# Kernel optimization log

Measured on AMD Instinct MI355X. Metric: run time of the kernel, lower is better.

## Reference

```python
import jax, jax.numpy as jnp
import numpy as np
import math

B, C, H, W = 8, 512, 32, 32
NUM_GROUPS = 32
NUM_HEADS = C // 64  # num_head_channels=64 -> 8 heads
EPS = 1e-5


def setup_inputs() -> dict:
    key = jax.random.key(0)
    ks = jax.random.split(key, 7)
    x = jax.random.normal(ks[0], (B, C, H, W), dtype=jnp.float32)
    gn_w = jax.random.uniform(ks[1], (C,), dtype=jnp.float32, minval=0.5, maxval=1.5)
    gn_b = jax.random.normal(ks[2], (C,), dtype=jnp.float32) * 0.1
    qkv_w = jax.random.normal(ks[3], (3 * C, C), dtype=jnp.float32) * 0.02
    qkv_b = jax.random.normal(ks[4], (3 * C,), dtype=jnp.float32) * 0.02
    proj_w = jax.random.normal(ks[5], (C, C), dtype=jnp.float32) * 0.02
    proj_b = jax.random.normal(ks[6], (C,), dtype=jnp.float32) * 0.02
    return {"x": x, "gn_w": gn_w, "gn_b": gn_b, "qkv_w": qkv_w,
            "qkv_b": qkv_b, "proj_w": proj_w, "proj_b": proj_b}


def _group_norm(x, w, b):
    # x: [B, C, L]
    bb, cc, ll = x.shape
    g = x.reshape(bb, NUM_GROUPS, cc // NUM_GROUPS, ll)
    mean = g.mean(axis=(2, 3), keepdims=True)
    var = g.var(axis=(2, 3), keepdims=True)
    g = (g - mean) * jax.lax.rsqrt(var + EPS)
    return g.reshape(bb, cc, ll) * w[None, :, None] + b[None, :, None]


def reference(x, gn_w, gn_b, qkv_w, qkv_b, proj_w, proj_b):
    b, c, h, w = x.shape
    L = h * w
    xf = x.reshape(b, c, L)
    # 1x1 conv1d QKV on normalized input: weight [3C, C]
    qkv = jnp.einsum('oc,bcl->bol', qkv_w, _group_norm(xf, gn_w, gn_b)) + qkv_b[None, :, None]
    ch = c // NUM_HEADS  # per-head channels
    qkv = qkv.reshape(b * NUM_HEADS, 3 * ch, L)
    q, k, v = qkv[:, :ch], qkv[:, ch:2 * ch], qkv[:, 2 * ch:]
    scale = 1.0 / math.sqrt(math.sqrt(ch))
    # [b*H, T, S] scores, softmax over source dim (computed in fp32 per source)
    weight = jnp.einsum('bct,bcs->bts', q * scale, k * scale)
    weight = jax.nn.softmax(weight.astype(jnp.float32), axis=-1).astype(weight.dtype)
    a = jnp.einsum('bts,bcs->bct', weight, v).reshape(b, c, L)
    hproj = jnp.einsum('oc,bcl->bol', proj_w, a) + proj_b[None, :, None]
    return (xf + hproj).reshape(b, c, h, w)
```

## Files before the change

### kernel.cpp

```cpp
#include <hip/hip_runtime.h>
#include <math.h>

#define BB 8
#define CC 512
#define LL 1024
#define GG 32
#define CPG 16
#define NH 8
#define CH 64

typedef unsigned short ushort_t;
typedef __attribute__((ext_vector_type(8))) short short8;
typedef __attribute__((ext_vector_type(4))) float f32x4;

#define SCALE_Q 0.18033688f

__device__ inline ushort_t f2bf(float f) {
  union { float f; unsigned u; } v;
  v.f = f;
  unsigned r = v.u + 0x7FFFu + ((v.u >> 16) & 1u);
  return (ushort_t)(r >> 16);
}

__device__ inline unsigned pack_bf2(float lo, float hi) {
  return __builtin_amdgcn_perm(__float_as_uint(hi), __float_as_uint(lo),
                               0x07060302u);
}

__device__ inline int swz(int r, int k) {
  return r * 64 + ((((k >> 3) ^ (r & 7)) << 3) | (k & 7));
}

__global__ __launch_bounds__(256) void gn_stats_kernel(
    const float* __restrict__ x, const float* __restrict__ gn_w,
    const float* __restrict__ gn_b, float* __restrict__ s_bc,
    float* __restrict__ t_bc) {
  int b = blockIdx.x / GG;
  int g = blockIdx.x % GG;
  const float* xg = x + ((size_t)b * CC + (size_t)g * CPG) * LL;
  float sum = 0.f, sq = 0.f;
  for (int i = threadIdx.x; i < CPG * LL; i += 256) {
    float v = xg[i];
    sum += v;
    sq += v * v;
  }
#pragma unroll
  for (int off = 32; off > 0; off >>= 1) {
    sum += __shfl_down(sum, off);
    sq += __shfl_down(sq, off);
  }
  __shared__ float red[8];
  __shared__ float st[2];
  int wave = threadIdx.x >> 6;
  if ((threadIdx.x & 63) == 0) {
    red[wave] = sum;
    red[4 + wave] = sq;
  }
  __syncthreads();
  if (threadIdx.x == 0) {
    float s = red[0] + red[1] + red[2] + red[3];
    float q = red[4] + red[5] + red[6] + red[7];
    float mean = s * (1.f / (CPG * LL));
    float var = q * (1.f / (CPG * LL)) - mean * mean;
    st[0] = mean;
    st[1] = rsqrtf(var + 1e-5f);
  }
  __syncthreads();
  if (threadIdx.x < CPG) {
    int c = g * CPG + threadIdx.x;
    float w = gn_w[c];
    float sc = st[1] * w;
    s_bc[b * CC + c] = sc;
    t_bc[b * CC + c] = gn_b[c] - st[0] * sc;
  }
}

__global__ __launch_bounds__(256) void convert_w_kernel(
    const float* __restrict__ qkv_w, const float* __restrict__ proj_w,
    ushort_t* __restrict__ wq, ushort_t* __restrict__ wp) {
  int idx = (blockIdx.x * 256 + threadIdx.x) * 4;
  const int N1 = 3 * CC * CC;
  float4 v;
  ushort_t* dst;
  if (idx < N1) {
    v = *(const float4*)(qkv_w + idx);
    dst = wq + idx;
  } else {
    int j = idx - N1;
    v = *(const float4*)(proj_w + j);
    dst = wp + j;
  }
  unsigned lo = f2bf(v.x) | ((unsigned)f2bf(v.y) << 16);
  unsigned hi = f2bf(v.z) | ((unsigned)f2bf(v.w) << 16);
  *(uint2*)dst = make_uint2(lo, hi);
}

__global__ __launch_bounds__(256) void xnt_kernel(
    const float* __restrict__ x, const float* __restrict__ s_bc,
    const float* __restrict__ t_bc, ushort_t* __restrict__ xnT) {
  const int b = blockIdx.z;
  const int c0 = blockIdx.y * 64;
  const int l0 = blockIdx.x * 64;
  const int tid = threadIdx.x;
  __shared__ ushort_t Ts[64 * 72];
#pragma unroll
  for (int r4 = 0; r4 < 4; ++r4) {
    int c_local = (tid >> 4) + r4 * 16;
    int l_local = (tid & 15) * 4;
    int c = c0 + c_local;
    float sc = s_bc[b * CC + c], sh = t_bc[b * CC + c];
    float4 v = *(const float4*)(x + ((size_t)b * CC + c) * LL + l0 + l_local);
    float vv[4] = {v.x, v.y, v.z, v.w};
#pragma unroll
    for (int dl = 0; dl < 4; ++dl) {
      int l = l_local + dl;
      int cs = c_local ^ (((l >> 2) & 7) << 3);
      Ts[l * 72 + cs] = f2bf(vv[dl] * sc + sh);
    }
  }
  __syncthreads();
#pragma unroll
  for (int rep = 0; rep < 2; ++rep) {
    int gid = tid + rep * 256;
    int l = gid >> 3, seg = gid & 7;
    uint4 v = *(const uint4*)&Ts[l * 72 + ((seg * 8) ^ (((l >> 2) & 7) << 3))];
    *(uint4*)(xnT + ((size_t)b * LL + l0 + l) * CC + c0 + seg * 8) = v;
  }
}

__global__ __launch_bounds__(256) void qkv_mfma_kernel(
    const ushort_t* __restrict__ wq, const ushort_t* __restrict__ xnT,
    const float* __restrict__ qkv_b, ushort_t* __restrict__ qT,
    ushort_t* __restrict__ kT, ushort_t* __restrict__ vbuf) {
  const int b = blockIdx.z;
  const int m0 = blockIdx.y * 128;
  const int n0 = blockIdx.x * 128;
  const int tid = threadIdx.x;
  const int w = tid >> 6, lane = tid & 63;
  const int col = lane & 15, quad = lane >> 4;
  const int wm = (w >> 1) * 64, wn = (w & 1) * 64;
  __shared__ ushort_t Smem[2 * 128 * 64];
  ushort_t* As = Smem;
  ushort_t* Bs = Smem + 128 * 64;
  f32x4 acc[4][4];
  f32x4 z = {0.f, 0.f, 0.f, 0.f};
#pragma unroll
  for (int i = 0; i < 4; ++i)
#pragma unroll
    for (int j = 0; j < 4; ++j) acc[i][j] = z;

  for (int k0 = 0; k0 < CC; k0 += 64) {
    __syncthreads();
#pragma unroll
    for (int rep = 0; rep < 4; ++rep) {
      int gid = tid + rep * 256;
      int r = gid >> 3, g = gid & 7;
      uint4 av = *(const uint4*)(wq + (size_t)(m0 + r) * CC + k0 + g * 8);
      *(uint4*)&As[swz(r, g * 8)] = av;
      uint4 bv =
          *(const uint4*)(xnT + ((size_t)b * LL + n0 + r) * CC + k0 + g * 8);
      *(uint4*)&Bs[swz(r, g * 8)] = bv;
    }
    __syncthreads();
#pragma unroll
    for (int kk = 0; kk < 2; ++kk) {
      short8 af[4], bf[4];
#pragma unroll
      for (int mi = 0; mi < 4; ++mi)
        af[mi] = *(const short8*)&As[swz(wm + mi * 16 + col, kk * 32 + quad * 8)];
#pragma unroll
      for (int ni = 0; ni < 4; ++ni)
        bf[ni] = *(const short8*)&Bs[swz(wn + ni * 16 + col, kk * 32 + quad * 8)];
#pragma unroll
      for (int mi = 0; mi < 4; ++mi)
#pragma unroll
        for (int ni = 0; ni < 4; ++ni)
          acc[mi][ni] = __builtin_amdgcn_mfma_f32_16x16x32_bf16(
              af[mi], bf[ni], acc[mi][ni], 0, 0, 0);
    }
  }
  __syncthreads();
  const int chunk_g = (m0 >> 6) + (w >> 1);
  const int sel = chunk_g % 3;
  ushort_t* Tile = Smem + (w >> 1) * 8192;
  if (sel < 2) {
    const float sc = (sel == 0) ? SCALE_Q : 1.f;
#pragma unroll
    for (int mi = 0; mi < 4; ++mi) {
      int mg = m0 + wm + mi * 16 + quad * 4;
      float b0 = qkv_b[mg + 0], b1 = qkv_b[mg + 1];
      float b2 = qkv_b[mg + 2], b3 = qkv_b[mg + 3];
      int ch = mi * 16 + quad * 4;
#pragma unroll
      for (int ni = 0; ni < 4; ++ni) {
        int lloc = wn + ni * 16 + col;
        float v0 = (acc[mi][ni][0] + b0) * sc;
        float v1 = (acc[mi][ni][1] + b1) * sc;
        float v2 = (acc[mi][ni][2] + b2) * sc;
        float v3 = (acc[mi][ni][3] + b3) * sc;
        int chs = ch ^ ((lloc & 7) << 3);
        *(uint2*)&Tile[lloc * 64 + chs] =
            make_uint2(pack_bf2(v0, v1), pack_bf2(v2, v3));
      }
    }
  } else {
#pragma unroll
    for (int mi = 0; mi < 4; ++mi)
#pragma unroll
      for (int r = 0; r < 4; ++r) {
        int ch = mi * 16 + quad * 4 + r;
        float bias = qkv_b[m0 + wm + ch];
#pragma unroll
        for (int ni = 0; ni < 4; ++ni) {
          int lloc = wn + ni * 16 + col;
          Tile[ch * 128 + lloc] =
              (ushort_t)(__float_as_uint(acc[mi][ni][r] + bias) >> 16);
        }
      }
  }
  __syncthreads();
#pragma unroll
  for (int ci = 0; ci < 2; ++ci) {
    int cg = (m0 >> 6) + ci;
    int head = cg / 3, sel2 = cg % 3;
    int bh = b * NH + head;
    ushort_t* T2 = Smem + ci * 8192;
    if (sel2 < 2) {
      ushort_t* dst = (sel2 == 0) ? qT : kT;
#pragma unroll
      for (int it = 0; it < 4; ++it) {
        int idx = tid + it * 256;
        int l = idx >> 3, seg = idx & 7;
        uint4 v = *(const uint4*)&T2[l * 64 + ((seg * 8) ^ ((l & 7) << 3))];
        *(uint4*)(dst + ((size_t)bh * LL + n0 + l) * CH + seg * 8) = v;
      }
    } else {
#pragma unroll
      for (int it = 0; it < 4; ++it) {
        int idx = tid + it * 256;
        int ch = idx >> 4, lseg = idx & 15;
        uint4 v = *(const uint4*)&T2[ch * 128 + lseg * 8];
        *(uint4*)(vbuf + ((size_t)bh * CH + ch) * LL + n0 + lseg * 8) = v;
      }
    }
  }
}

__global__ __launch_bounds__(256) void attn_mfma_kernel(
    const ushort_t* __restrict__ qT, const ushort_t* __restrict__ kT,
    const ushort_t* __restrict__ vbuf, ushort_t* __restrict__ abuf) {
  const int B = blockIdx.x;
  const int bh = (B & 7) * 8 + ((B >> 3) >> 4);
  const int t0g = ((B >> 3) & 15) * 64;
  const int b = bh >> 3, h = bh & 7;
  const int tid = threadIdx.x;
  const int w = tid >> 6, lane = tid & 63;
  const int col = lane & 15, quad = lane >> 4;
  const int strip = w * 16;
  __shared__ ushort_t QPs[64 * 64];
  __shared__ ushort_t Ks[64 * 64];
  __shared__ ushort_t Vs[64 * 64];

#pragma unroll
  for (int rep = 0; rep < 2; ++rep) {
    int gid = tid + rep * 256;
    int r = gid >> 3, g = gid & 7;
    uint4 v = *(const uint4*)(qT + ((size_t)bh * LL + t0g + r) * CH + g * 8);
    *(uint4*)&QPs[swz(r, g * 8)] = v;
  }
  __syncthreads();
  short8 bq[2];
  bq[0] = *(const short8*)&QPs[swz(strip + col, quad * 8)];
  bq[1] = *(const short8*)&QPs[swz(strip + col, 32 + quad * 8)];

  float m_s = 0.f, lsum = 0.f;
  f32x4 oacc[4];
  f32x4 z = {0.f, 0.f, 0.f, 0.f};
#pragma unroll
  for (int ci = 0; ci < 4; ++ci) oacc[ci] = z;

  for (int s0 = 0; s0 < LL; s0 += 64) {
    __syncthreads();
#pragma unroll
    for (int rep = 0; rep < 2; ++rep) {
      int gid = tid + rep * 256;
      int r = gid >> 3, g = gid & 7;
      uint4 kv = *(const uint4*)(kT + ((size_t)bh * LL + s0 + r) * CH + g * 8);
      *(uint4*)&Ks[swz(r, g * 8)] = kv;
      uint4 vv = *(const uint4*)(vbuf + ((size_t)bh * CH + r) * LL + s0 + g * 8);
      *(uint4*)&Vs[swz(r, g * 8)] = vv;
    }
    __syncthreads();
    f32x4 sacc[4];
#pragma unroll
    for (int si = 0; si < 4; ++si) sacc[si] = z;
#pragma unroll
    for (int kk = 0; kk < 2; ++kk)
#pragma unroll
      for (int si = 0; si < 4; ++si) {
        short8 ak = *(const short8*)&Ks[swz(si * 16 + col, kk * 32 + quad * 8)];
        sacc[si] = __builtin_amdgcn_mfma_f32_16x16x32_bf16(ak, bq[kk], sacc[si], 0, 0, 0);
      }
    if (s0 == 0) {
      float mx = sacc[0][0];
#pragma unroll
      for (int si = 0; si < 4; ++si)
#pragma unroll
        for (int r = 0; r < 4; ++r) mx = fmaxf(mx, sacc[si][r]);
      mx = fmaxf(mx, __shfl_xor(mx, 16));
      mx = fmaxf(mx, __shfl_xor(mx, 32));
      m_s = mx;
    }
#pragma unroll
    for (int si = 0; si < 4; ++si) {
      float p0 = __builtin_amdgcn_exp2f(sacc[si][0] - m_s);
      float p1 = __builtin_amdgcn_exp2f(sacc[si][1] - m_s);
      float p2 = __builtin_amdgcn_exp2f(sacc[si][2] - m_s);
      float p3 = __builtin_amdgcn_exp2f(sacc[si][3] - m_s);
      lsum += (p0 + p1) + (p2 + p3);
      int base = swz(strip + col, si * 16 + quad * 4);
      *(unsigned*)&QPs[base] = pack_bf2(p0, p1);
      *(unsigned*)&QPs[base + 2] = pack_bf2(p2, p3);
    }
#pragma unroll
    for (int kk = 0; kk < 2; ++kk) {
      short8 ap = *(const short8*)&QPs[swz(strip + col, kk * 32 + quad * 8)];
#pragma unroll
      for (int ci = 0; ci < 4; ++ci) {
        short8 bv = *(const short8*)&Vs[swz(ci * 16 + col, kk * 32 + quad * 8)];
        oacc[ci] = __builtin_amdgcn_mfma_f32_16x16x32_bf16(ap, bv, oacc[ci], 0, 0, 0);
      }
    }
  }
  lsum += __shfl_xor(lsum, 16);
  lsum += __shfl_xor(lsum, 32);
  float linv[4];
#pragma unroll
  for (int r = 0; r < 4; ++r)
    linv[r] = 1.f / __shfl(lsum, (lane & 48) | (quad * 4 + r), 64);
#pragma unroll
  for (int r = 0; r < 4; ++r) {
    int l = t0g + strip + quad * 4 + r;
#pragma unroll
    for (int ci = 0; ci < 4; ++ci) {
      int c = h * CH + ci * 16 + col;
      abuf[((size_t)b * LL + l) * CC + c] = f2bf(oacc[ci][r] * linv[r]);
    }
  }
}

__global__ __launch_bounds__(256) void proj_mfma_kernel(
    const ushort_t* __restrict__ wp, const ushort_t* __restrict__ abuf,
    const float* __restrict__ proj_b, const float* __restrict__ x,
    float* __restrict__ out) {
  const int b = blockIdx.z;
  const int m0 = blockIdx.y * 64;
  const int n0 = blockIdx.x * 128;
  const int tid = threadIdx.x;
  const int w = tid >> 6, lane = tid & 63;
  const int col = lane & 15, quad = lane >> 4;
  const int wm = (w >> 1) * 32, wn = (w & 1) * 64;
  __shared__ ushort_t As[64 * 64];
  __shared__ ushort_t Bs[128 * 64];
  f32x4 acc[2][4];
  f32x4 z = {0.f, 0.f, 0.f, 0.f};
#pragma unroll
  for (int i = 0; i < 2; ++i)
#pragma unroll
    for (int j = 0; j < 4; ++j) acc[i][j] = z;

  for (int k0 = 0; k0 < CC; k0 += 64) {
    __syncthreads();
#pragma unroll
    for (int rep = 0; rep < 2; ++rep) {
      int idx = tid + rep * 256;
      int r = idx >> 3, g = idx & 7;
      uint4 av = *(const uint4*)(wp + (size_t)(m0 + r) * CC + k0 + g * 8);
      *(uint4*)&As[swz(r, g * 8)] = av;
    }
#pragma unroll
    for (int rep = 0; rep < 4; ++rep) {
      int idx = tid + rep * 256;
      int r = idx >> 3, g = idx & 7;
      uint4 bv =
          *(const uint4*)(abuf + ((size_t)b * LL + n0 + r) * CC + k0 + g * 8);
      *(uint4*)&Bs[swz(r, g * 8)] = bv;
    }
    __syncthreads();
#pragma unroll
    for (int kk = 0; kk < 2; ++kk) {
      short8 af[2], bf[4];
#pragma unroll
      for (int mi = 0; mi < 2; ++mi)
        af[mi] = *(const short8*)&As[swz(wm + mi * 16 + col, kk * 32 + quad * 8)];
#pragma unroll
      for (int ni = 0; ni < 4; ++ni)
        bf[ni] = *(const short8*)&Bs[swz(wn + ni * 16 + col, kk * 32 + quad * 8)];
#pragma unroll
      for (int mi = 0; mi < 2; ++mi)
#pragma unroll
        for (int ni = 0; ni < 4; ++ni)
          acc[mi][ni] = __builtin_amdgcn_mfma_f32_16x16x32_bf16(
              af[mi], bf[ni], acc[mi][ni], 0, 0, 0);
    }
  }
#pragma unroll
  for (int mi = 0; mi < 2; ++mi)
#pragma unroll
    for (int r = 0; r < 4; ++r) {
      int o = m0 + wm + mi * 16 + quad * 4 + r;
      float bias = proj_b[o];
#pragma unroll
      for (int ni = 0; ni < 4; ++ni) {
        int l = n0 + wn + ni * 16 + col;
        size_t off = ((size_t)b * CC + o) * LL + l;
        out[off] = x[off] + bias + acc[mi][ni][r];
      }
    }
}

extern "C" void kernel_launch(void* const* d_in, const int* in_sizes, int n_in,
                              void* d_out, int out_size, void* d_ws,
                              size_t ws_size, hipStream_t stream) {
  const float* x = (const float*)d_in[0];
  const float* gn_w = (const float*)d_in[1];
  const float* gn_b = (const float*)d_in[2];
  const float* qkv_w = (const float*)d_in[3];
  const float* qkv_b = (const float*)d_in[4];
  const float* proj_w = (const float*)d_in[5];
  const float* proj_b = (const float*)d_in[6];
  float* out = (float*)d_out;

  char* ws = (char*)d_ws;
  float* s_bc = (float*)ws;
  float* t_bc = s_bc + BB * CC;
  ushort_t* wq = (ushort_t*)(t_bc + BB * CC);
  ushort_t* wp = wq + (size_t)3 * CC * CC;
  ushort_t* xnT = wp + (size_t)CC * CC;
  ushort_t* qT = xnT + (size_t)BB * LL * CC;
  ushort_t* kT = qT + (size_t)BB * NH * LL * CH;
  ushort_t* vb = kT + (size_t)BB * NH * LL * CH;
  ushort_t* abuf = vb + (size_t)BB * NH * LL * CH;

  gn_stats_kernel<<<BB * GG, 256, 0, stream>>>(x, gn_w, gn_b, s_bc, t_bc);
  convert_w_kernel<<<1024, 256, 0, stream>>>(qkv_w, proj_w, wq, wp);
  xnt_kernel<<<dim3(LL / 64, CC / 64, BB), 256, 0, stream>>>(x, s_bc, t_bc,
                                                             xnT);
  qkv_mfma_kernel<<<dim3(LL / 128, (3 * CC) / 128, BB), 256, 0, stream>>>(
      wq, xnT, qkv_b, qT, kT, vb);
  attn_mfma_kernel<<<dim3(1024), 256, 0, stream>>>(qT, kT, vb, abuf);
  proj_mfma_kernel<<<dim3(LL / 128, CC / 64, BB), 256, 0, stream>>>(
      wp, abuf, proj_b, x, out);
}
```

Measured before the change: 170.8 us.

## Pre-swizzle global layouts and use direct global-to-LDS loads with K/V double buffering

Weights, xnT, kT/vbuf and abuf are now written to global memory already in the XOR-swizzled order the LDS tiles expect. The GEMMs and attention can then stage tiles with global_load_lds 16-byte copies instead of going through registers. The attention kernel double-buffers its K/V tiles so the next tile's load overlaps the MFMA work, reads Q fragments straight from global memory, and raises wave priority around the MFMA sections. GroupNorm stats and weight conversion are merged into one launch. The cost is a tighter coupling between global layouts and swizzle conventions, which is easy to get wrong.

```diff
diff --git a/kernel.cpp b/kernel.cpp
--- a/kernel.cpp
+++ b/kernel.cpp
@@ -31,68 +31,82 @@
   return r * 64 + ((((k >> 3) ^ (r & 7)) << 3) | (k & 7));
 }
 
-__global__ __launch_bounds__(256) void gn_stats_kernel(
+__device__ __forceinline__ void g2l16(const void* g, void* l) {
+  __builtin_amdgcn_global_load_lds((const unsigned int*)g, (unsigned int*)l,
+                                   16, 0, 0);
+}
+
+__global__ __launch_bounds__(256) void pre_kernel(
     const float* __restrict__ x, const float* __restrict__ gn_w,
-    const float* __restrict__ gn_b, float* __restrict__ s_bc,
-    float* __restrict__ t_bc) {
-  int b = blockIdx.x / GG;
-  int g = blockIdx.x % GG;
-  const float* xg = x + ((size_t)b * CC + (size_t)g * CPG) * LL;
-  float sum = 0.f, sq = 0.f;
-  for (int i = threadIdx.x; i < CPG * LL; i += 256) {
-    float v = xg[i];
-    sum += v;
-    sq += v * v;
-  }
-#pragma unroll
-  for (int off = 32; off > 0; off >>= 1) {
-    sum += __shfl_down(sum, off);
-    sq += __shfl_down(sq, off);
-  }
-  __shared__ float red[8];
-  __shared__ float st[2];
-  int wave = threadIdx.x >> 6;
-  if ((threadIdx.x & 63) == 0) {
-    red[wave] = sum;
-    red[4 + wave] = sq;
-  }
-  __syncthreads();
-  if (threadIdx.x == 0) {
-    float s = red[0] + red[1] + red[2] + red[3];
-    float q = red[4] + red[5] + red[6] + red[7];
-    float mean = s * (1.f / (CPG * LL));
-    float var = q * (1.f / (CPG * LL)) - mean * mean;
-    st[0] = mean;
-    st[1] = rsqrtf(var + 1e-5f);
-  }
-  __syncthreads();
-  if (threadIdx.x < CPG) {
-    int c = g * CPG + threadIdx.x;
-    float w = gn_w[c];
-    float sc = st[1] * w;
-    s_bc[b * CC + c] = sc;
-    t_bc[b * CC + c] = gn_b[c] - st[0] * sc;
-  }
-}
-
-__global__ __launch_bounds__(256) void convert_w_kernel(
-    const float* __restrict__ qkv_w, const float* __restrict__ proj_w,
-    ushort_t* __restrict__ wq, ushort_t* __restrict__ wp) {
-  int idx = (blockIdx.x * 256 + threadIdx.x) * 4;
-  const int N1 = 3 * CC * CC;
-  float4 v;
-  ushort_t* dst;
-  if (idx < N1) {
-    v = *(const float4*)(qkv_w + idx);
-    dst = wq + idx;
+    const float* __restrict__ gn_b, const float* __restrict__ qkv_w,
+    const float* __restrict__ proj_w, float* __restrict__ s_bc,
+    float* __restrict__ t_bc, ushort_t* __restrict__ wq,
+    ushort_t* __restrict__ wp) {
+  if (blockIdx.x < BB * GG) {
+    int b = blockIdx.x / GG;
+    int g = blockIdx.x % GG;
+    const float4* xg4 =
+        (const float4*)(x + ((size_t)b * CC + (size_t)g * CPG) * LL);
+    float sum = 0.f, sq = 0.f;
+#pragma unroll
+    for (int i = 0; i < 16; ++i) {
+      float4 v = xg4[threadIdx.x + i * 256];
+      sum += (v.x + v.y) + (v.z + v.w);
+      sq += (v.x * v.x + v.y * v.y) + (v.z * v.z + v.w * v.w);
+    }
+#pragma unroll
+    for (int off = 32; off > 0; off >>= 1) {
+      sum += __shfl_down(sum, off);
+      sq += __shfl_down(sq, off);
+    }
+    __shared__ float red[8];
+    __shared__ float st[2];
+    int wave = threadIdx.x >> 6;
+    if ((threadIdx.x & 63) == 0) {
+      red[wave] = sum;
+      red[4 + wave] = sq;
+    }
+    __syncthreads();
+    if (threadIdx.x == 0) {
+      float s = red[0] + red[1] + red[2] + red[3];
+      float q = red[4] + red[5] + red[6] + red[7];
+      float mean = s * (1.f / (CPG * LL));
+      float var = q * (1.f / (CPG * LL)) - mean * mean;
+      st[0] = mean;
+      st[1] = rsqrtf(var + 1e-5f);
+    }
+    __syncthreads();
+    if (threadIdx.x < CPG) {
+      int c = g * CPG + threadIdx.x;
+      float w = gn_w[c];
+      float sc = st[1] * w;
+      s_bc[b * CC + c] = sc;
+      t_bc[b * CC + c] = gn_b[c] - st[0] * sc;
+    }
   } else {
-    int j = idx - N1;
-    v = *(const float4*)(proj_w + j);
-    dst = wp + j;
-  }
-  unsigned lo = f2bf(v.x) | ((unsigned)f2bf(v.y) << 16);
-  unsigned hi = f2bf(v.z) | ((unsigned)f2bf(v.w) << 16);
-  *(uint2*)dst = make_uint2(lo, hi);
+    int cb = blockIdx.x - BB * GG;
+    int idx = (cb * 256 + threadIdx.x) * 4;
+    const int N1 = 3 * CC * CC;
+    float4 v;
+    ushort_t* mat;
+    int row, k;
+    if (idx < N1) {
+      v = *(const float4*)(qkv_w + idx);
+      row = idx >> 9;
+      k = idx & 511;
+      mat = wq + (size_t)row * CC;
+    } else {
+      int j = idx - N1;
+      v = *(const float4*)(proj_w + j);
+      row = j >> 9;
+      k = j & 511;
+      mat = wp + (size_t)row * CC;
+    }
+    int dcol = (k & ~63) | ((((k >> 3) & 7) ^ (row & 7)) << 3) | (k & 7);
+    unsigned lo = f2bf(v.x) | ((unsigned)f2bf(v.y) << 16);
+    unsigned hi = f2bf(v.z) | ((unsigned)f2bf(v.w) << 16);
+    *(uint2*)(mat + dcol) = make_uint2(lo, hi);
+  }
 }
 
 __global__ __launch_bounds__(256) void xnt_kernel(
@@ -124,7 +138,8 @@
     int gid = tid + rep * 256;
     int l = gid >> 3, seg = gid & 7;
     uint4 v = *(const uint4*)&Ts[l * 72 + ((seg * 8) ^ (((l >> 2) & 7) << 3))];
-    *(uint4*)(xnT + ((size_t)b * LL + l0 + l) * CC + c0 + seg * 8) = v;
+    *(uint4*)(xnT + ((size_t)b * LL + l0 + l) * CC + c0 +
+              ((seg ^ (l & 7)) << 3)) = v;
   }
 }
 
@@ -149,17 +164,18 @@
 #pragma unroll
     for (int j = 0; j < 4; ++j) acc[i][j] = z;
 
+  const ushort_t* arow = wq + (size_t)m0 * CC;
+  const ushort_t* brow = xnT + ((size_t)b * LL + n0) * CC;
+  const int eb = w * 2048 + lane * 8;
+
   for (int k0 = 0; k0 < CC; k0 += 64) {
     __syncthreads();
 #pragma unroll
-    for (int rep = 0; rep < 4; ++rep) {
-      int gid = tid + rep * 256;
-      int r = gid >> 3, g = gid & 7;
-      uint4 av = *(const uint4*)(wq + (size_t)(m0 + r) * CC + k0 + g * 8);
-      *(uint4*)&As[swz(r, g * 8)] = av;
-      uint4 bv =
-          *(const uint4*)(xnT + ((size_t)b * LL + n0 + r) * CC + k0 + g * 8);
-      *(uint4*)&Bs[swz(r, g * 8)] = bv;
+    for (int i = 0; i < 4; ++i) {
+      int ee = eb + i * 512;
+      int r = ee >> 6, c = ee & 63;
+      g2l16(arow + (size_t)r * CC + k0 + c, As + (w * 2048 + i * 512));
+      g2l16(brow + (size_t)r * CC + k0 + c, Bs + (w * 2048 + i * 512));
     }
     __syncthreads();
 #pragma unroll
@@ -231,8 +247,9 @@
       for (int it = 0; it < 4; ++it) {
         int idx = tid + it * 256;
         int l = idx >> 3, seg = idx & 7;
-        uint4 v = *(const uint4*)&T2[l * 64 + ((seg * 8) ^ ((l & 7) << 3))];
-        *(uint4*)(dst + ((size_t)bh * LL + n0 + l) * CH + seg * 8) = v;
+        uint4 v = *(const uint4*)&T2[l * 64 + seg * 8];
+        *(uint4*)(dst + ((size_t)bh * LL + n0 + l) * CC / 8 * 0 +
+                  ((size_t)bh * LL + n0 + l) * CH + seg * 8) = v;
       }
     } else {
 #pragma unroll
@@ -240,7 +257,9 @@
         int idx = tid + it * 256;
         int ch = idx >> 4, lseg = idx & 15;
         uint4 v = *(const uint4*)&T2[ch * 128 + lseg * 8];
-        *(uint4*)(vbuf + ((size_t)bh * CH + ch) * LL + n0 + lseg * 8) = v;
+        int g = lseg & 7, blk = lseg >> 3;
+        *(uint4*)(vbuf + ((size_t)bh * CH + ch) * LL + n0 + blk * 64 +
+                  ((g ^ (ch & 7)) << 3)) = v;
       }
     }
   }
@@ -249,59 +268,70 @@
 __global__ __launch_bounds__(256) void attn_mfma_kernel(
     const ushort_t* __restrict__ qT, const ushort_t* __restrict__ kT,
     const ushort_t* __restrict__ vbuf, ushort_t* __restrict__ abuf) {
-  const int B = blockIdx.x;
-  const int bh = (B & 7) * 8 + ((B >> 3) >> 4);
-  const int t0g = ((B >> 3) & 15) * 64;
+  const int Bx = blockIdx.x;
+  const int bh = (Bx & 7) * 8 + ((Bx >> 3) >> 4);
+  const int t0g = ((Bx >> 3) & 15) * 64;
   const int b = bh >> 3, h = bh & 7;
   const int tid = threadIdx.x;
   const int w = tid >> 6, lane = tid & 63;
   const int col = lane & 15, quad = lane >> 4;
   const int strip = w * 16;
-  __shared__ ushort_t QPs[64 * 64];
-  __shared__ ushort_t Ks[64 * 64];
-  __shared__ ushort_t Vs[64 * 64];
-
-#pragma unroll
-  for (int rep = 0; rep < 2; ++rep) {
-    int gid = tid + rep * 256;
-    int r = gid >> 3, g = gid & 7;
-    uint4 v = *(const uint4*)(qT + ((size_t)bh * LL + t0g + r) * CH + g * 8);
-    *(uint4*)&QPs[swz(r, g * 8)] = v;
-  }
-  __syncthreads();
+  __shared__ ushort_t Ps[64 * 64];
+  __shared__ ushort_t Ksm[2][64 * 64];
+  __shared__ ushort_t Vsm[2][64 * 64];
+
+  const ushort_t* kbase = kT + (size_t)bh * LL * CH;
+  const ushort_t* vbase = vbuf + (size_t)bh * CH * LL;
+  const int eb = w * 1024 + lane * 8;
+
+#pragma unroll
+  for (int i = 0; i < 2; ++i) {
+    int ee = eb + i * 512;
+    g2l16(kbase + ee, &Ksm[0][w * 1024 + i * 512]);
+    g2l16(vbase + (size_t)(ee >> 6) * LL + (ee & 63),
+          &Vsm[0][w * 1024 + i * 512]);
+  }
+  const ushort_t* qtile = qT + ((size_t)bh * LL + t0g) * CH;
   short8 bq[2];
-  bq[0] = *(const short8*)&QPs[swz(strip + col, quad * 8)];
-  bq[1] = *(const short8*)&QPs[swz(strip + col, 32 + quad * 8)];
+  bq[0] = *(const short8*)&qtile[swz(strip + col, quad * 8)];
+  bq[1] = *(const short8*)&qtile[swz(strip + col, 32 + quad * 8)];
 
   float m_s = 0.f, lsum = 0.f;
   f32x4 oacc[4];
   f32x4 z = {0.f, 0.f, 0.f, 0.f};
 #pragma unroll
   for (int ci = 0; ci < 4; ++ci) oacc[ci] = z;
-
-  for (int s0 = 0; s0 < LL; s0 += 64) {
-    __syncthreads();
-#pragma unroll
-    for (int rep = 0; rep < 2; ++rep) {
-      int gid = tid + rep * 256;
-      int r = gid >> 3, g = gid & 7;
-      uint4 kv = *(const uint4*)(kT + ((size_t)bh * LL + s0 + r) * CH + g * 8);
-      *(uint4*)&Ks[swz(r, g * 8)] = kv;
-      uint4 vv = *(const uint4*)(vbuf + ((size_t)bh * CH + r) * LL + s0 + g * 8);
-      *(uint4*)&Vs[swz(r, g * 8)] = vv;
-    }
-    __syncthreads();
+  __syncthreads();
+
+  int cur = 0;
+  for (int it = 0; it < 16; ++it) {
+    if (it < 15) {
+      const ushort_t* kn = kbase + (size_t)(it + 1) * 64 * CH;
+      const ushort_t* vn = vbase + (it + 1) * 64;
+#pragma unroll
+      for (int i = 0; i < 2; ++i) {
+        int ee = eb + i * 512;
+        g2l16(kn + ee, &Ksm[cur ^ 1][w * 1024 + i * 512]);
+        g2l16(vn + (size_t)(ee >> 6) * LL + (ee & 63),
+              &Vsm[cur ^ 1][w * 1024 + i * 512]);
+      }
+    }
+    const ushort_t* Kc = Ksm[cur];
+    const ushort_t* Vc = Vsm[cur];
     f32x4 sacc[4];
 #pragma unroll
     for (int si = 0; si < 4; ++si) sacc[si] = z;
+    __builtin_amdgcn_s_setprio(1);
 #pragma unroll
     for (int kk = 0; kk < 2; ++kk)
 #pragma unroll
       for (int si = 0; si < 4; ++si) {
-        short8 ak = *(const short8*)&Ks[swz(si * 16 + col, kk * 32 + quad * 8)];
-        sacc[si] = __builtin_amdgcn_mfma_f32_16x16x32_bf16(ak, bq[kk], sacc[si], 0, 0, 0);
-      }
-    if (s0 == 0) {
+        short8 ak = *(const short8*)&Kc[swz(si * 16 + col, kk * 32 + quad * 8)];
+        sacc[si] = __builtin_amdgcn_mfma_f32_16x16x32_bf16(ak, bq[kk],
+                                                           sacc[si], 0, 0, 0);
+      }
+    __builtin_amdgcn_s_setprio(0);
+    if (it == 0) {
       float mx = sacc[0][0];
 #pragma unroll
       for (int si = 0; si < 4; ++si)
@@ -319,18 +349,23 @@
       float p3 = __builtin_amdgcn_exp2f(sacc[si][3] - m_s);
       lsum += (p0 + p1) + (p2 + p3);
       int base = swz(strip + col, si * 16 + quad * 4);
-      *(unsigned*)&QPs[base] = pack_bf2(p0, p1);
-      *(unsigned*)&QPs[base + 2] = pack_bf2(p2, p3);
-    }
+      *(unsigned*)&Ps[base] = pack_bf2(p0, p1);
+      *(unsigned*)&Ps[base + 2] = pack_bf2(p2, p3);
+    }
+    __builtin_amdgcn_s_setprio(1);
 #pragma unroll
     for (int kk = 0; kk < 2; ++kk) {
-      short8 ap = *(const short8*)&QPs[swz(strip + col, kk * 32 + quad * 8)];
+      short8 ap = *(const short8*)&Ps[swz(strip + col, kk * 32 + quad * 8)];
 #pragma unroll
       for (int ci = 0; ci < 4; ++ci) {
-        short8 bv = *(const short8*)&Vs[swz(ci * 16 + col, kk * 32 + quad * 8)];
-        oacc[ci] = __builtin_amdgcn_mfma_f32_16x16x32_bf16(ap, bv, oacc[ci], 0, 0, 0);
-      }
-    }
+        short8 bv = *(const short8*)&Vc[swz(ci * 16 + col, kk * 32 + quad * 8)];
+        oacc[ci] = __builtin_amdgcn_mfma_f32_16x16x32_bf16(ap, bv, oacc[ci],
+                                                           0, 0, 0);
+      }
+    }
+    __builtin_amdgcn_s_setprio(0);
+    __syncthreads();
+    cur ^= 1;
   }
   lsum += __shfl_xor(lsum, 16);
   lsum += __shfl_xor(lsum, 32);
@@ -343,8 +378,10 @@
     int l = t0g + strip + quad * 4 + r;
 #pragma unroll
     for (int ci = 0; ci < 4; ++ci) {
-      int c = h * CH + ci * 16 + col;
-      abuf[((size_t)b * LL + l) * CC + c] = f2bf(oacc[ci][r] * linv[r]);
+      int cl = ci * 16 + col;
+      int dcol = ((((cl >> 3) ^ (l & 7)) << 3) | (cl & 7));
+      abuf[((size_t)b * LL + l) * CC + h * CH + dcol] =
+          f2bf(oacc[ci][r] * linv[r]);
     }
   }
 }
@@ -369,22 +406,24 @@
 #pragma unroll
     for (int j = 0; j < 4; ++j) acc[i][j] = z;
 
+  const ushort_t* arow = wp + (size_t)m0 * CC;
+  const ushort_t* brow = abuf + ((size_t)b * LL + n0) * CC;
+  const int ea = w * 1024 + lane * 8;
+  const int ebb = w * 2048 + lane * 8;
+
   for (int k0 = 0; k0 < CC; k0 += 64) {
     __syncthreads();
 #pragma unroll
-    for (int rep = 0; rep < 2; ++rep) {
-      int idx = tid + rep * 256;
-      int r = idx >> 3, g = idx & 7;
-      uint4 av = *(const uint4*)(wp + (size_t)(m0 + r) * CC + k0 + g * 8);
-      *(uint4*)&As[swz(r, g * 8)] = av;
-    }
-#pragma unroll
-    for (int rep = 0; rep < 4; ++rep) {
-      int idx = tid + rep * 256;
-      int r = idx >> 3, g = idx & 7;
-      uint4 bv =
-          *(const uint4*)(abuf + ((size_t)b * LL + n0 + r) * CC + k0 + g * 8);
-      *(uint4*)&Bs[swz(r, g * 8)] = bv;
+    for (int i = 0; i < 2; ++i) {
+      int ee = ea + i * 512;
+      g2l16(arow + (size_t)(ee >> 6) * CC + k0 + (ee & 63),
+            As + (w * 1024 + i * 512));
+    }
+#pragma unroll
+    for (int i = 0; i < 4; ++i) {
+      int ee = ebb + i * 512;
+      g2l16(brow + (size_t)(ee >> 6) * CC + k0 + (ee & 63),
+            Bs + (w * 2048 + i * 512));
     }
     __syncthreads();
 #pragma unroll
@@ -442,8 +481,8 @@
   ushort_t* vb = kT + (size_t)BB * NH * LL * CH;
   ushort_t* abuf = vb + (size_t)BB * NH * LL * CH;
 
-  gn_stats_kernel<<<BB * GG, 256, 0, stream>>>(x, gn_w, gn_b, s_bc, t_bc);
-  convert_w_kernel<<<1024, 256, 0, stream>>>(qkv_w, proj_w, wq, wp);
+  pre_kernel<<<BB * GG + 1024, 256, 0, stream>>>(x, gn_w, gn_b, qkv_w, proj_w,
+                                                 s_bc, t_bc, wq, wp);
   xnt_kernel<<<dim3(LL / 64, CC / 64, BB), 256, 0, stream>>>(x, s_bc, t_bc,
                                                              xnT);
   qkv_mfma_kernel<<<dim3(LL / 128, (3 * CC) / 128, BB), 256, 0, stream>>>(
```

Measured after the change: 151.1 us. 11.5% less time.
